# Optimization experiments

Measured on AMD Instinct MI355X. Metric: run time of the kernel, lower is better.

The kernel has to match this reference:

```python
import jax, jax.numpy as jnp
import numpy as np

NUM_EXPERTS = 8
HIDDEN = 2048
INTER = 4096
TOKENS = 8192
TOP_K = 2


def setup_inputs() -> dict:
    key = jax.random.key(0)
    ks = jax.random.split(key, 5)
    s = 0.02
    return {
        "x": jax.random.normal(ks[0], (TOKENS, HIDDEN), dtype=jnp.float32),
        "gate_w": jax.random.normal(ks[1], (NUM_EXPERTS, HIDDEN), dtype=jnp.float32) * s,
        "w1": jax.random.normal(ks[2], (NUM_EXPERTS, INTER, HIDDEN), dtype=jnp.float32) * s,
        "w2": jax.random.normal(ks[3], (NUM_EXPERTS, HIDDEN, INTER), dtype=jnp.float32) * s,
        "w3": jax.random.normal(ks[4], (NUM_EXPERTS, INTER, HIDDEN), dtype=jnp.float32) * s,
    }


def reference(x, gate_w, w1, w2, w3):
    # Router: softmax over experts in fp32, then top-2 (no renormalization,
    # matching the torch module which uses the raw top-k softmax probs).
    router_logits = jnp.einsum("th,eh->te", x, gate_w)  # [T, E]
    probs = jax.nn.softmax(router_logits.astype(jnp.float32), axis=1)
    topk_w, topk_idx = jax.lax.top_k(probs, TOP_K)  # [T, K]
    topk_w = topk_w.astype(x.dtype)

    num_experts = w1.shape[0]
    out = jnp.zeros_like(x)
    for e in range(num_experts):
        # Combined routing coefficient for expert e per token (0 if unrouted).
        coef = jnp.sum(jnp.where(topk_idx == e, topk_w, 0.0), axis=1)  # [T]
        # SwiGLU expert FFN: down(silu(gate(x)) * up(x))
        g = jnp.einsum("th,ih->ti", x, w1[e])
        u = jnp.einsum("th,ih->ti", x, w3[e])
        h = jax.nn.silu(g) * u
        y = jnp.einsum("ti,hi->th", h, w2[e])
        out = out + coef[:, None] * y
    return out
```

## Files before the change

kernel.cpp:

```cpp
#include <hip/hip_runtime.h>
#include <stdint.h>
#include <stddef.h>


constexpr int kTokens  = 8192;
constexpr int kHidden  = 2048;
constexpr int kInter   = 4096;
constexpr int kExperts = 8;

constexpr int BM = 128;
constexpr int BN = 128;
constexpr int BK = 64;
constexpr int MAX_MT = (2 * kTokens) / BM + kExperts;

typedef short bf16x8 __attribute__((ext_vector_type(8)));
typedef float f32x4  __attribute__((ext_vector_type(4)));
typedef unsigned int u32;

__device__ __forceinline__ unsigned short f2bf(float f) {
  union { float f; unsigned u; } v; v.f = f;
  unsigned r = v.u + 0x7FFFu + ((v.u >> 16) & 1u);
  return (unsigned short)(r >> 16);
}

__device__ __forceinline__ void gload16(const void* g, void* l) {
  __builtin_amdgcn_global_load_lds(
      (const __attribute__((address_space(1))) u32*)g,
      (__attribute__((address_space(3))) u32*)l, 16, 0, 0);
}

__global__ __launch_bounds__(256) void convert_w(
    const float* __restrict__ src, unsigned short* __restrict__ dst,
    int lp, int lq, int K, long nchunks)
{
  long stride = (long)gridDim.x * blockDim.x;
  for (long g = blockIdx.x * (long)blockDim.x + threadIdx.x; g < nchunks; g += stride) {
    int  l   = (int)(g & 1023);
    long blk = g >> 10;
    int  q   = (int)(blk & ((1 << lq) - 1));
    long ep  = blk >> lq;
    int  p   = (int)(ep & ((1 << lp) - 1));
    int  e   = (int)(ep >> lp);
    int r = l >> 3, cs = l & 7, c = cs ^ (r & 7);
    size_t soff = (((size_t)(e << lp) + p) * 128 + r) * (size_t)K + (size_t)q * 64 + c * 8;
    float4 v0 = *reinterpret_cast<const float4*>(src + soff);
    float4 v1 = *reinterpret_cast<const float4*>(src + soff + 4);
    uint4 o;
    o.x = (u32)f2bf(v0.x) | ((u32)f2bf(v0.y) << 16);
    o.y = (u32)f2bf(v0.z) | ((u32)f2bf(v0.w) << 16);
    o.z = (u32)f2bf(v1.x) | ((u32)f2bf(v1.y) << 16);
    o.w = (u32)f2bf(v1.z) | ((u32)f2bf(v1.w) << 16);
    *reinterpret_cast<uint4*>(dst + g * 8) = o;
  }
}

__global__ __launch_bounds__(256) void moe_router(
    const float* __restrict__ x, const float* __restrict__ gate_w,
    unsigned short* __restrict__ xb, int* __restrict__ counts,
    int* __restrict__ list_idx, float* __restrict__ list_w)
{
  const int lane = threadIdx.x & 63;
  const int wave = threadIdx.x >> 6;
  const int t = blockIdx.x * 4 + wave;

  float acc[kExperts];
#pragma unroll
  for (int e = 0; e < kExperts; ++e) acc[e] = 0.f;

  const float4* xrow = reinterpret_cast<const float4*>(x + (size_t)t * kHidden);
#pragma unroll
  for (int j = 0; j < 8; ++j) {
    float4 xv = xrow[j * 64 + lane];
    uint2 pk;
    pk.x = (u32)f2bf(xv.x) | ((u32)f2bf(xv.y) << 16);
    pk.y = (u32)f2bf(xv.z) | ((u32)f2bf(xv.w) << 16);
    *reinterpret_cast<uint2*>(xb + (size_t)t * kHidden + j * 256 + lane * 4) = pk;
#pragma unroll
    for (int e = 0; e < kExperts; ++e) {
      float4 gv = reinterpret_cast<const float4*>(gate_w + (size_t)e * kHidden)[j * 64 + lane];
      acc[e] += xv.x * gv.x + xv.y * gv.y + xv.z * gv.z + xv.w * gv.w;
    }
  }
#pragma unroll
  for (int e = 0; e < kExperts; ++e) {
#pragma unroll
    for (int m = 32; m >= 1; m >>= 1) acc[e] += __shfl_xor(acc[e], m);
  }
  if (lane == 0) {
    float mx = acc[0];
#pragma unroll
    for (int e = 1; e < kExperts; ++e) mx = fmaxf(mx, acc[e]);
    float p[kExperts]; float s = 0.f;
#pragma unroll
    for (int e = 0; e < kExperts; ++e) { p[e] = __expf(acc[e] - mx); s += p[e]; }
    float inv = 1.f / s;
    int i1 = 0; float v1 = p[0];
#pragma unroll
    for (int e = 1; e < kExperts; ++e) if (p[e] > v1) { v1 = p[e]; i1 = e; }
    int i2 = (i1 == 0) ? 1 : 0; float v2 = p[i2];
#pragma unroll
    for (int e = 0; e < kExperts; ++e) {
      if (e == i1 || e == i2) continue;
      if (p[e] > v2) { v2 = p[e]; i2 = e; }
    }
    int s1 = atomicAdd(&counts[i1], 1);
    list_idx[i1 * kTokens + s1] = t;
    list_w [i1 * kTokens + s1] = v1 * inv;
    int s2 = atomicAdd(&counts[i2], 1);
    list_idx[i2 * kTokens + s2] = t;
    list_w [i2 * kTokens + s2] = v2 * inv;
  }
}

__device__ __forceinline__ bool map_tile(const int* __restrict__ counts, int mt,
                                         int& e, int& lm, int& sb, int& ne)
{
  int tb = 0; sb = 0;
  for (e = 0; e < kExperts; ++e) {
    ne = counts[e];
    int tiles = (ne + BM - 1) / BM;
    if (mt < tb + tiles) { lm = mt - tb; return true; }
    tb += tiles; sb += ne;
  }
  return false;
}

__global__ __launch_bounds__(256, 2) void moe_gu(
    const unsigned short* __restrict__ xb,
    const unsigned short* __restrict__ w1b, const unsigned short* __restrict__ w3b,
    const int* __restrict__ counts, const int* __restrict__ list_idx,
    unsigned short* __restrict__ hbuf)
{
  __shared__ unsigned short As [BM * BK];
  __shared__ unsigned short B1s[BN * BK];
  __shared__ unsigned short B3s[BN * BK];
  __shared__ int toks[BM];

  const int tid = threadIdx.x;
  const int nt  = blockIdx.x / MAX_MT;
  const int mt  = blockIdx.x % MAX_MT;

  int e, lm, sb, ne;
  if (!map_tile(counts, mt, e, lm, sb, ne)) return;
  const int row0 = lm * BM;

  if (tid < BM) {
    int lr = row0 + tid;
    toks[tid] = list_idx[e * kTokens + ((lr < ne) ? lr : 0)];
  }
  __syncthreads();

  const int lane = tid & 63;
  const int w = tid >> 6;
  const int wr = w >> 1, wc = w & 1;

  const unsigned short* srcA[4];
  const unsigned short* srcB1[4];
  const unsigned short* srcB3[4];
  const size_t bbase = ((size_t)(e * (kInter / BN) + nt) * (kHidden / BK)) * 1024;
#pragma unroll
  for (int i = 0; i < 4; ++i) {
    int l = (w * 4 + i) * 64 + lane;
    int r = l >> 3, cs = l & 7, c = cs ^ (r & 7);
    srcA[i]  = xb  + (size_t)toks[r] * kHidden + c * 8;
    srcB1[i] = w1b + (bbase + l) * 8;
    srcB3[i] = w3b + (bbase + l) * 8;
  }

  f32x4 accG[4][4], accU[4][4];
  const f32x4 zero = {0.f, 0.f, 0.f, 0.f};
#pragma unroll
  for (int m = 0; m < 4; ++m)
#pragma unroll
    for (int n = 0; n < 4; ++n) { accG[m][n] = zero; accU[m][n] = zero; }

  for (int ks = 0; ks < kHidden / BK; ++ks) {
#pragma unroll
    for (int i = 0; i < 4; ++i) {
      gload16(srcA[i]  + ks * BK,            &As [(w * 4 + i) * 512]);
      gload16(srcB1[i] + (size_t)ks * 8192,  &B1s[(w * 4 + i) * 512]);
      gload16(srcB3[i] + (size_t)ks * 8192,  &B3s[(w * 4 + i) * 512]);
    }
    __syncthreads();
#pragma unroll
    for (int kk = 0; kk < 2; ++kk) {
      const int cq = kk * 4 + (lane >> 4);
      bf16x8 a[4], b1v[4], b3v[4];
#pragma unroll
      for (int m = 0; m < 4; ++m) {
        int row = wr * 64 + m * 16 + (lane & 15);
        a[m] = *reinterpret_cast<const bf16x8*>(&As[row * 64 + ((cq ^ (row & 7)) << 3)]);
      }
#pragma unroll
      for (int n = 0; n < 4; ++n) {
        int row = wc * 64 + n * 16 + (lane & 15);
        b1v[n] = *reinterpret_cast<const bf16x8*>(&B1s[row * 64 + ((cq ^ (row & 7)) << 3)]);
        b3v[n] = *reinterpret_cast<const bf16x8*>(&B3s[row * 64 + ((cq ^ (row & 7)) << 3)]);
      }
#pragma unroll
      for (int m = 0; m < 4; ++m)
#pragma unroll
        for (int n = 0; n < 4; ++n) {
          accG[m][n] = __builtin_amdgcn_mfma_f32_16x16x32_bf16(a[m], b1v[n], accG[m][n], 0, 0, 0);
          accU[m][n] = __builtin_amdgcn_mfma_f32_16x16x32_bf16(a[m], b3v[n], accU[m][n], 0, 0, 0);
        }
    }
    __syncthreads();
  }

#pragma unroll
  for (int m = 0; m < 4; ++m) {
#pragma unroll
    for (int r = 0; r < 4; ++r) {
      int rloc = wr * 64 + m * 16 + ((lane >> 4) * 4) + r;
      int lrow = row0 + rloc;
      if (lrow < ne) {
        size_t base = (size_t)(sb + lrow) * kInter + (size_t)nt * BN + wc * 64 + (lane & 15);
#pragma unroll
        for (int n = 0; n < 4; ++n) {
          float g = accG[m][n][r];
          float u = accU[m][n][r];
          float hv = (g / (1.f + __expf(-g))) * u;
          hbuf[base + n * 16] = f2bf(hv);
        }
      }
    }
  }
}

__global__ __launch_bounds__(256, 3) void moe_y(
    const unsigned short* __restrict__ hbuf,
    const unsigned short* __restrict__ w2b,
    const int* __restrict__ counts, const int* __restrict__ list_idx,
    const float* __restrict__ list_w,
    float* __restrict__ out)
{
  __shared__ unsigned short As[BM * BK];
  __shared__ unsigned short Bs[BN * BK];
  __shared__ int   toks[BM];
  __shared__ float cofs[BM];

  const int tid = threadIdx.x;
  const int nt  = blockIdx.x / MAX_MT;
  const int mt  = blockIdx.x % MAX_MT;

  int e, lm, sb, ne;
  if (!map_tile(counts, mt, e, lm, sb, ne)) return;
  const int row0 = lm * BM;

  if (tid < BM) {
    int lr = row0 + tid;
    bool v = lr < ne;
    toks[tid] = v ? list_idx[e * kTokens + lr] : 0;
    cofs[tid] = v ? list_w [e * kTokens + lr] : 0.f;
  }
  __syncthreads();

  const int lane = tid & 63;
  const int w = tid >> 6;
  const int wr = w >> 1, wc = w & 1;

  const unsigned short* srcA[4];
  const unsigned short* srcB2[4];
  const size_t bbase = ((size_t)(e * (kHidden / BN) + nt) * (kInter / BK)) * 1024;
#pragma unroll
  for (int i = 0; i < 4; ++i) {
    int l = (w * 4 + i) * 64 + lane;
    int r = l >> 3, cs = l & 7, c = cs ^ (r & 7);
    srcA[i]  = hbuf + (size_t)(sb + row0 + r) * kInter + c * 8;
    srcB2[i] = w2b  + (bbase + l) * 8;
  }

  f32x4 acc[4][4];
  const f32x4 zero = {0.f, 0.f, 0.f, 0.f};
#pragma unroll
  for (int m = 0; m < 4; ++m)
#pragma unroll
    for (int n = 0; n < 4; ++n) acc[m][n] = zero;

  for (int ks = 0; ks < kInter / BK; ++ks) {
#pragma unroll
    for (int i = 0; i < 4; ++i) {
      gload16(srcA[i]  + ks * BK,           &As[(w * 4 + i) * 512]);
      gload16(srcB2[i] + (size_t)ks * 8192, &Bs[(w * 4 + i) * 512]);
    }
    __syncthreads();
#pragma unroll
    for (int kk = 0; kk < 2; ++kk) {
      const int cq = kk * 4 + (lane >> 4);
      bf16x8 a[4], b[4];
#pragma unroll
      for (int m = 0; m < 4; ++m) {
        int row = wr * 64 + m * 16 + (lane & 15);
        a[m] = *reinterpret_cast<const bf16x8*>(&As[row * 64 + ((cq ^ (row & 7)) << 3)]);
      }
#pragma unroll
      for (int n = 0; n < 4; ++n) {
        int row = wc * 64 + n * 16 + (lane & 15);
        b[n] = *reinterpret_cast<const bf16x8*>(&Bs[row * 64 + ((cq ^ (row & 7)) << 3)]);
      }
#pragma unroll
      for (int m = 0; m < 4; ++m)
#pragma unroll
        for (int n = 0; n < 4; ++n)
          acc[m][n] = __builtin_amdgcn_mfma_f32_16x16x32_bf16(a[m], b[n], acc[m][n], 0, 0, 0);
    }
    __syncthreads();
  }

#pragma unroll
  for (int m = 0; m < 4; ++m) {
#pragma unroll
    for (int r = 0; r < 4; ++r) {
      int rloc = wr * 64 + m * 16 + ((lane >> 4) * 4) + r;
      if (row0 + rloc < ne) {
        float cf = cofs[rloc];
        size_t obase = (size_t)toks[rloc] * kHidden + (size_t)nt * BN + wc * 64 + (lane & 15);
#pragma unroll
        for (int n = 0; n < 4; ++n)
          atomicAdd(&out[obase + n * 16], cf * acc[m][n][r]);
      }
    }
  }
}

__global__ __launch_bounds__(256, 2) void moe_gu_f32(
    const unsigned short* __restrict__ xb,
    const float* __restrict__ w1, const float* __restrict__ w3,
    const int* __restrict__ counts, const int* __restrict__ list_idx,
    unsigned short* __restrict__ hbuf)
{
  __shared__ unsigned short As [BM * BK];
  __shared__ unsigned short B1s[BN * BK];
  __shared__ unsigned short B3s[BN * BK];
  __shared__ int toks[BM];

  const int tid = threadIdx.x;
  const int nt  = blockIdx.x / MAX_MT;
  const int mt  = blockIdx.x % MAX_MT;

  int e, lm, sb, ne;
  if (!map_tile(counts, mt, e, lm, sb, ne)) return;
  const int row0 = lm * BM;

  if (tid < BM) {
    int lr = row0 + tid;
    toks[tid] = list_idx[e * kTokens + ((lr < ne) ? lr : 0)];
  }
  __syncthreads();

  const unsigned short* aptr[4];
#pragma unroll
  for (int i = 0; i < 4; ++i) {
    int chunk = i * 256 + tid;
    int r = chunk >> 3, c8 = chunk & 7;
    aptr[i] = xb + (size_t)toks[r] * kHidden + c8 * 8;
  }
  const float* w1e = w1 + (size_t)e * kInter * kHidden;
  const float* w3e = w3 + (size_t)e * kInter * kHidden;

  f32x4 accG[4][4], accU[4][4];
  const f32x4 zero = {0.f, 0.f, 0.f, 0.f};
#pragma unroll
  for (int m = 0; m < 4; ++m)
#pragma unroll
    for (int n = 0; n < 4; ++n) { accG[m][n] = zero; accU[m][n] = zero; }

  const int lane = tid & 63;
  const int wr = (tid >> 6) >> 1;
  const int wc = (tid >> 6) & 1;

  for (int k0 = 0; k0 < kHidden; k0 += BK) {
#pragma unroll
    for (int i = 0; i < 4; ++i) {
      int chunk = i * 256 + tid;
      uint4 v = *reinterpret_cast<const uint4*>(aptr[i] + k0);
      *reinterpret_cast<uint4*>(&As[chunk * 8]) = v;
    }
#pragma unroll
    for (int i = 0; i < 8; ++i) {
      int c = i * 256 + tid;
      int rowB = c >> 4, c16 = c & 15;
      size_t off = ((size_t)(nt * BN + rowB)) * kHidden + k0 + c16 * 4;
      float4 v1 = *reinterpret_cast<const float4*>(w1e + off);
      float4 v3 = *reinterpret_cast<const float4*>(w3e + off);
      uint2 p1, p3;
      p1.x = (u32)f2bf(v1.x) | ((u32)f2bf(v1.y) << 16);
      p1.y = (u32)f2bf(v1.z) | ((u32)f2bf(v1.w) << 16);
      p3.x = (u32)f2bf(v3.x) | ((u32)f2bf(v3.y) << 16);
      p3.y = (u32)f2bf(v3.z) | ((u32)f2bf(v3.w) << 16);
      *reinterpret_cast<uint2*>(&B1s[rowB * BK + c16 * 4]) = p1;
      *reinterpret_cast<uint2*>(&B3s[rowB * BK + c16 * 4]) = p3;
    }
    __syncthreads();
#pragma unroll
    for (int kk = 0; kk < 2; ++kk) {
      const int klo = kk * 32 + (lane >> 4) * 8;
      bf16x8 a[4], b1v[4], b3v[4];
#pragma unroll
      for (int m = 0; m < 4; ++m)
        a[m] = *reinterpret_cast<const bf16x8*>(&As[(wr * 64 + m * 16 + (lane & 15)) * BK + klo]);
#pragma unroll
      for (int n = 0; n < 4; ++n) {
        b1v[n] = *reinterpret_cast<const bf16x8*>(&B1s[(wc * 64 + n * 16 + (lane & 15)) * BK + klo]);
        b3v[n] = *reinterpret_cast<const bf16x8*>(&B3s[(wc * 64 + n * 16 + (lane & 15)) * BK + klo]);
      }
#pragma unroll
      for (int m = 0; m < 4; ++m)
#pragma unroll
        for (int n = 0; n < 4; ++n) {
          accG[m][n] = __builtin_amdgcn_mfma_f32_16x16x32_bf16(a[m], b1v[n], accG[m][n], 0, 0, 0);
          accU[m][n] = __builtin_amdgcn_mfma_f32_16x16x32_bf16(a[m], b3v[n], accU[m][n], 0, 0, 0);
        }
    }
    __syncthreads();
  }
#pragma unroll
  for (int m = 0; m < 4; ++m) {
#pragma unroll
    for (int r = 0; r < 4; ++r) {
      int rloc = wr * 64 + m * 16 + ((lane >> 4) * 4) + r;
      int lrow = row0 + rloc;
      if (lrow < ne) {
        size_t base = (size_t)(sb + lrow) * kInter + (size_t)nt * BN + wc * 64 + (lane & 15);
#pragma unroll
        for (int n = 0; n < 4; ++n) {
          float g = accG[m][n][r];
          float u = accU[m][n][r];
          hbuf[base + n * 16] = f2bf((g / (1.f + __expf(-g))) * u);
        }
      }
    }
  }
}

__global__ __launch_bounds__(256, 2) void moe_y_f32(
    const unsigned short* __restrict__ hbuf,
    const float* __restrict__ w2,
    const int* __restrict__ counts, const int* __restrict__ list_idx,
    const float* __restrict__ list_w,
    float* __restrict__ out)
{
  __shared__ unsigned short As[BM * BK];
  __shared__ unsigned short Bs[BN * BK];
  __shared__ int   toks[BM];
  __shared__ float cofs[BM];

  const int tid = threadIdx.x;
  const int nt  = blockIdx.x / MAX_MT;
  const int mt  = blockIdx.x % MAX_MT;

  int e, lm, sb, ne;
  if (!map_tile(counts, mt, e, lm, sb, ne)) return;
  const int row0 = lm * BM;

  if (tid < BM) {
    int lr = row0 + tid;
    bool v = lr < ne;
    toks[tid] = v ? list_idx[e * kTokens + lr] : 0;
    cofs[tid] = v ? list_w [e * kTokens + lr] : 0.f;
  }
  __syncthreads();

  const float* w2e = w2 + (size_t)e * kHidden * kInter;
  const unsigned short* arow = hbuf + (size_t)(sb + row0) * kInter;

  f32x4 acc[4][4];
  const f32x4 zero = {0.f, 0.f, 0.f, 0.f};
#pragma unroll
  for (int m = 0; m < 4; ++m)
#pragma unroll
    for (int n = 0; n < 4; ++n) acc[m][n] = zero;

  const int lane = tid & 63;
  const int wr = (tid >> 6) >> 1;
  const int wc = (tid >> 6) & 1;

  for (int k0 = 0; k0 < kInter; k0 += BK) {
#pragma unroll
    for (int i = 0; i < 4; ++i) {
      int chunk = i * 256 + tid;
      int r = chunk >> 3, c8 = chunk & 7;
      uint4 v = *reinterpret_cast<const uint4*>(arow + (size_t)r * kInter + k0 + c8 * 8);
      *reinterpret_cast<uint4*>(&As[chunk * 8]) = v;
    }
#pragma unroll
    for (int i = 0; i < 8; ++i) {
      int c = i * 256 + tid;
      int rowB = c >> 4, c16 = c & 15;
      size_t off = ((size_t)(nt * BN + rowB)) * kInter + k0 + c16 * 4;
      float4 v2 = *reinterpret_cast<const float4*>(w2e + off);
      uint2 p2;
      p2.x = (u32)f2bf(v2.x) | ((u32)f2bf(v2.y) << 16);
      p2.y = (u32)f2bf(v2.z) | ((u32)f2bf(v2.w) << 16);
      *reinterpret_cast<uint2*>(&Bs[rowB * BK + c16 * 4]) = p2;
    }
    __syncthreads();
#pragma unroll
    for (int kk = 0; kk < 2; ++kk) {
      const int klo = kk * 32 + (lane >> 4) * 8;
      bf16x8 a[4], b[4];
#pragma unroll
      for (int m = 0; m < 4; ++m)
        a[m] = *reinterpret_cast<const bf16x8*>(&As[(wr * 64 + m * 16 + (lane & 15)) * BK + klo]);
#pragma unroll
      for (int n = 0; n < 4; ++n)
        b[n] = *reinterpret_cast<const bf16x8*>(&Bs[(wc * 64 + n * 16 + (lane & 15)) * BK + klo]);
#pragma unroll
      for (int m = 0; m < 4; ++m)
#pragma unroll
        for (int n = 0; n < 4; ++n)
          acc[m][n] = __builtin_amdgcn_mfma_f32_16x16x32_bf16(a[m], b[n], acc[m][n], 0, 0, 0);
    }
    __syncthreads();
  }
#pragma unroll
  for (int m = 0; m < 4; ++m) {
#pragma unroll
    for (int r = 0; r < 4; ++r) {
      int rloc = wr * 64 + m * 16 + ((lane >> 4) * 4) + r;
      if (row0 + rloc < ne) {
        float cf = cofs[rloc];
        size_t obase = (size_t)toks[rloc] * kHidden + (size_t)nt * BN + wc * 64 + (lane & 15);
#pragma unroll
        for (int n = 0; n < 4; ++n)
          atomicAdd(&out[obase + n * 16], cf * acc[m][n][r]);
      }
    }
  }
}

extern "C" void kernel_launch(void* const* d_in, const int* in_sizes, int n_in,
                              void* d_out, int out_size, void* d_ws, size_t ws_size,
                              hipStream_t stream)
{
  const float* x      = (const float*)d_in[0];
  const float* gate_w = (const float*)d_in[1];
  const float* w1     = (const float*)d_in[2];
  const float* w2     = (const float*)d_in[3];
  const float* w3     = (const float*)d_in[4];
  float* out = (float*)d_out;

  char* ws = (char*)d_ws;
  const size_t MiB = 1ull << 20;
  int*   counts   = (int*)(ws);
  int*   list_idx = (int*)(ws + 1024);
  float* list_w   = (float*)(ws + 1024 + kExperts * kTokens * 4);

  hipMemsetAsync(counts, 0, 1024, stream);
  hipMemsetAsync(out, 0, (size_t)kTokens * kHidden * sizeof(float), stream);

  if (ws_size >= 418 * MiB) {
    unsigned short* xb   = (unsigned short*)(ws + 1 * MiB);
    unsigned short* w1b  = (unsigned short*)(ws + 33 * MiB);
    unsigned short* w3b  = (unsigned short*)(ws + 161 * MiB);
    unsigned short* hbuf = (unsigned short*)(ws + 289 * MiB);
    unsigned short* w2b  = w1b;

    const long nch = (long)kExperts * (kInter / BN) * (kHidden / BK) * 1024;
    convert_w<<<4096, 256, 0, stream>>>(w1, w1b, 5, 5, kHidden, nch);
    convert_w<<<4096, 256, 0, stream>>>(w3, w3b, 5, 5, kHidden, nch);
    moe_router<<<kTokens / 4, 256, 0, stream>>>(x, gate_w, xb, counts, list_idx, list_w);
    moe_gu<<<(kInter / BN) * MAX_MT, 256, 0, stream>>>(xb, w1b, w3b, counts, list_idx, hbuf);
    convert_w<<<4096, 256, 0, stream>>>(w2, w2b, 4, 6, kInter, nch);
    moe_y<<<(kHidden / BN) * MAX_MT, 256, 0, stream>>>(hbuf, w2b, counts, list_idx, list_w, out);
  } else {
    unsigned short* xb   = (unsigned short*)(ws + 1 * MiB);
    unsigned short* hbuf = (unsigned short*)(ws + 36 * MiB);
    moe_router<<<kTokens / 4, 256, 0, stream>>>(x, gate_w, xb, counts, list_idx, list_w);
    moe_gu_f32<<<(kInter / BN) * MAX_MT, 256, 0, stream>>>(xb, w1, w3, counts, list_idx, hbuf);
    moe_y_f32 <<<(kHidden / BN) * MAX_MT, 256, 0, stream>>>(hbuf, w2, counts, list_idx, list_w, out);
  }
}
```

Baseline: 1.498 ms.

## Rewrite gate/up GEMM as 256-row tile, 8-wave double-buffered ping-pong kernel

Replaces the gate/up expert GEMM with a 512-thread kernel that uses 256x128 tiles and double-buffers A, W1 and W3 tiles in 128KB of LDS. Global-to-LDS loads for the next K step are interleaved with MFMA phases, using s_setprio, explicit vmcnt waits and split barriers. The aim is to hide load latency and raise arithmetic intensity per block. The cost is higher LDS use, which limits occupancy, and tail waste on smaller per-expert tiles. The fine-grained waitcnt counts must stay correct.

```diff
diff --git a/kernel.cpp b/kernel.cpp
--- a/kernel.cpp
+++ b/kernel.cpp
@@ -8,10 +8,12 @@
 constexpr int kInter   = 4096;
 constexpr int kExperts = 8;
 
-constexpr int BM = 128;
-constexpr int BN = 128;
-constexpr int BK = 64;
+constexpr int BM = 128, BN = 128, BK = 64;
 constexpr int MAX_MT = (2 * kTokens) / BM + kExperts;
+
+constexpr int BM2 = 256, BN2 = 128, BK2 = 64;
+constexpr int MAX_MT2 = (2 * kTokens) / BM2 + kExperts;
+constexpr int NT2 = kHidden / BK2;
 
 typedef short bf16x8 __attribute__((ext_vector_type(8)));
 typedef float f32x4  __attribute__((ext_vector_type(4)));
@@ -125,101 +127,207 @@
   return false;
 }
 
-__global__ __launch_bounds__(256, 2) void moe_gu(
+__device__ __forceinline__ bool map_tile2(const int* __restrict__ counts, int mt,
+                                          int& e, int& lm, int& sb, int& ne)
+{
+  int tb = 0; sb = 0;
+  for (e = 0; e < kExperts; ++e) {
+    ne = counts[e];
+    int tiles = (ne + BM2 - 1) / BM2;
+    if (mt < tb + tiles) { lm = mt - tb; return true; }
+    tb += tiles; sb += ne;
+  }
+  return false;
+}
+
+__global__ __launch_bounds__(512, 2) void moe_gu2(
     const unsigned short* __restrict__ xb,
     const unsigned short* __restrict__ w1b, const unsigned short* __restrict__ w3b,
     const int* __restrict__ counts, const int* __restrict__ list_idx,
     unsigned short* __restrict__ hbuf)
 {
-  __shared__ unsigned short As [BM * BK];
-  __shared__ unsigned short B1s[BN * BK];
-  __shared__ unsigned short B3s[BN * BK];
-  __shared__ int toks[BM];
+  __shared__ unsigned short lds[65536];
+  __shared__ int toks[BM2];
 
   const int tid = threadIdx.x;
-  const int nt  = blockIdx.x / MAX_MT;
-  const int mt  = blockIdx.x % MAX_MT;
+  const int nt  = blockIdx.x / MAX_MT2;
+  const int mt  = blockIdx.x % MAX_MT2;
 
   int e, lm, sb, ne;
-  if (!map_tile(counts, mt, e, lm, sb, ne)) return;
-  const int row0 = lm * BM;
-
-  if (tid < BM) {
+  if (!map_tile2(counts, mt, e, lm, sb, ne)) return;
+  const int row0 = lm * BM2;
+
+  if (tid < BM2) {
     int lr = row0 + tid;
     toks[tid] = list_idx[e * kTokens + ((lr < ne) ? lr : 0)];
   }
   __syncthreads();
 
   const int lane = tid & 63;
-  const int w = tid >> 6;
-  const int wr = w >> 1, wc = w & 1;
-
-  const unsigned short* srcA[4];
-  const unsigned short* srcB1[4];
-  const unsigned short* srcB3[4];
-  const size_t bbase = ((size_t)(e * (kInter / BN) + nt) * (kHidden / BK)) * 1024;
-#pragma unroll
-  for (int i = 0; i < 4; ++i) {
-    int l = (w * 4 + i) * 64 + lane;
-    int r = l >> 3, cs = l & 7, c = cs ^ (r & 7);
-    srcA[i]  = xb  + (size_t)toks[r] * kHidden + c * 8;
-    srcB1[i] = w1b + (bbase + l) * 8;
-    srcB3[i] = w3b + (bbase + l) * 8;
-  }
-
-  f32x4 accG[4][4], accU[4][4];
+  const int w    = tid >> 6;
+  const int wr   = w >> 2;
+  const int wc   = w & 3;
+
+  const unsigned short* srcA[2][2];
+  const unsigned short* srcB1[2];
+  const unsigned short* srcB3[2];
+  {
+    const size_t bb = ((size_t)(e * (kInter / BN2) + nt) * (kHidden / BK2)) * 1024;
+#pragma unroll
+    for (int i = 0; i < 2; ++i) {
+      int l = (w * 2 + i) * 64 + lane;
+      int r = l >> 3, cs = l & 7, c = cs ^ (r & 7);
+#pragma unroll
+      for (int h = 0; h < 2; ++h)
+        srcA[h][i] = xb + (size_t)toks[h * 128 + r] * kHidden + c * 8;
+      srcB1[i] = w1b + (bb + l) * 8;
+      srcB3[i] = w3b + (bb + l) * 8;
+    }
+  }
+
+  f32x4 accG[8][2], accU[8][2];
   const f32x4 zero = {0.f, 0.f, 0.f, 0.f};
 #pragma unroll
-  for (int m = 0; m < 4; ++m)
-#pragma unroll
-    for (int n = 0; n < 4; ++n) { accG[m][n] = zero; accU[m][n] = zero; }
-
-  for (int ks = 0; ks < kHidden / BK; ++ks) {
-#pragma unroll
-    for (int i = 0; i < 4; ++i) {
-      gload16(srcA[i]  + ks * BK,            &As [(w * 4 + i) * 512]);
-      gload16(srcB1[i] + (size_t)ks * 8192,  &B1s[(w * 4 + i) * 512]);
-      gload16(srcB3[i] + (size_t)ks * 8192,  &B3s[(w * 4 + i) * 512]);
-    }
-    __syncthreads();
-#pragma unroll
-    for (int kk = 0; kk < 2; ++kk) {
-      const int cq = kk * 4 + (lane >> 4);
-      bf16x8 a[4], b1v[4], b3v[4];
+  for (int m = 0; m < 8; ++m)
+#pragma unroll
+    for (int n = 0; n < 2; ++n) { accG[m][n] = zero; accU[m][n] = zero; }
+
+#pragma unroll
+  for (int i = 0; i < 2; ++i) gload16(srcA[0][i], &lds[0 * 8192 + (w * 2 + i) * 512]);
+#pragma unroll
+  for (int i = 0; i < 2; ++i) gload16(srcA[1][i], &lds[1 * 8192 + (w * 2 + i) * 512]);
+#pragma unroll
+  for (int i = 0; i < 2; ++i) gload16(srcB1[i], &lds[32768 + (w * 2 + i) * 512]);
+#pragma unroll
+  for (int i = 0; i < 2; ++i) gload16(srcB3[i], &lds[49152 + (w * 2 + i) * 512]);
+  asm volatile("s_waitcnt vmcnt(2)" ::: "memory");
+  __builtin_amdgcn_sched_barrier(0);
+  __builtin_amdgcn_s_barrier();
+
+  for (int t = 0; t < NT2; ++t) {
+    const int cb = t & 1, nb = cb ^ 1;
+    const int tn = (t + 1 < NT2) ? (t + 1) : (NT2 - 1);
+    const int Acur = (cb * 2 + wr) * 8192;
+    const int B1c  = 32768 + cb * 8192;
+    const int B3c  = 49152 + cb * 8192;
+    const int An0  = (nb * 2 + 0) * 8192;
+    const int An1  = (nb * 2 + 1) * 8192;
+    const int B1n  = 32768 + nb * 8192;
+    const int B3n  = 49152 + nb * 8192;
+
+    bf16x8 a0[4][2], a1[4][2];
+    {
+      bf16x8 b1f[2][2];
 #pragma unroll
       for (int m = 0; m < 4; ++m) {
-        int row = wr * 64 + m * 16 + (lane & 15);
-        a[m] = *reinterpret_cast<const bf16x8*>(&As[row * 64 + ((cq ^ (row & 7)) << 3)]);
-      }
-#pragma unroll
-      for (int n = 0; n < 4; ++n) {
-        int row = wc * 64 + n * 16 + (lane & 15);
-        b1v[n] = *reinterpret_cast<const bf16x8*>(&B1s[row * 64 + ((cq ^ (row & 7)) << 3)]);
-        b3v[n] = *reinterpret_cast<const bf16x8*>(&B3s[row * 64 + ((cq ^ (row & 7)) << 3)]);
-      }
-#pragma unroll
-      for (int m = 0; m < 4; ++m)
-#pragma unroll
-        for (int n = 0; n < 4; ++n) {
-          accG[m][n] = __builtin_amdgcn_mfma_f32_16x16x32_bf16(a[m], b1v[n], accG[m][n], 0, 0, 0);
-          accU[m][n] = __builtin_amdgcn_mfma_f32_16x16x32_bf16(a[m], b3v[n], accU[m][n], 0, 0, 0);
+        const int r = m * 16 + (lane & 15);
+#pragma unroll
+        for (int kk = 0; kk < 2; ++kk) {
+          const int cq = kk * 4 + (lane >> 4);
+          a0[m][kk] = *reinterpret_cast<const bf16x8*>(&lds[Acur + r * 64 + ((cq ^ (r & 7)) << 3)]);
         }
-    }
-    __syncthreads();
-  }
-
-#pragma unroll
-  for (int m = 0; m < 4; ++m) {
+      }
+#pragma unroll
+      for (int n = 0; n < 2; ++n) {
+        const int r = wc * 32 + n * 16 + (lane & 15);
+#pragma unroll
+        for (int kk = 0; kk < 2; ++kk) {
+          const int cq = kk * 4 + (lane >> 4);
+          b1f[n][kk] = *reinterpret_cast<const bf16x8*>(&lds[B1c + r * 64 + ((cq ^ (r & 7)) << 3)]);
+        }
+      }
+#pragma unroll
+      for (int i = 0; i < 2; ++i) gload16(srcA[0][i] + tn * 64, &lds[An0 + (w * 2 + i) * 512]);
+      __builtin_amdgcn_s_setprio(1);
+#pragma unroll
+      for (int m = 0; m < 4; ++m)
+#pragma unroll
+        for (int n = 0; n < 2; ++n)
+#pragma unroll
+          for (int kk = 0; kk < 2; ++kk)
+            accG[m][n] = __builtin_amdgcn_mfma_f32_16x16x32_bf16(a0[m][kk], b1f[n][kk], accG[m][n], 0, 0, 0);
+      __builtin_amdgcn_s_setprio(0);
+      __builtin_amdgcn_sched_barrier(0);
+      __builtin_amdgcn_s_barrier();
+
+#pragma unroll
+      for (int m = 0; m < 4; ++m) {
+        const int r = 64 + m * 16 + (lane & 15);
+#pragma unroll
+        for (int kk = 0; kk < 2; ++kk) {
+          const int cq = kk * 4 + (lane >> 4);
+          a1[m][kk] = *reinterpret_cast<const bf16x8*>(&lds[Acur + r * 64 + ((cq ^ (r & 7)) << 3)]);
+        }
+      }
+#pragma unroll
+      for (int i = 0; i < 2; ++i) gload16(srcA[1][i] + tn * 64, &lds[An1 + (w * 2 + i) * 512]);
+      __builtin_amdgcn_s_setprio(1);
+#pragma unroll
+      for (int m = 0; m < 4; ++m)
+#pragma unroll
+        for (int n = 0; n < 2; ++n)
+#pragma unroll
+          for (int kk = 0; kk < 2; ++kk)
+            accG[4 + m][n] = __builtin_amdgcn_mfma_f32_16x16x32_bf16(a1[m][kk], b1f[n][kk], accG[4 + m][n], 0, 0, 0);
+      __builtin_amdgcn_s_setprio(0);
+      __builtin_amdgcn_sched_barrier(0);
+      asm volatile("s_waitcnt vmcnt(4)" ::: "memory");
+      __builtin_amdgcn_s_barrier();
+    }
+    {
+      bf16x8 b3f[2][2];
+#pragma unroll
+      for (int n = 0; n < 2; ++n) {
+        const int r = wc * 32 + n * 16 + (lane & 15);
+#pragma unroll
+        for (int kk = 0; kk < 2; ++kk) {
+          const int cq = kk * 4 + (lane >> 4);
+          b3f[n][kk] = *reinterpret_cast<const bf16x8*>(&lds[B3c + r * 64 + ((cq ^ (r & 7)) << 3)]);
+        }
+      }
+#pragma unroll
+      for (int i = 0; i < 2; ++i) gload16(srcB1[i] + (size_t)tn * 8192, &lds[B1n + (w * 2 + i) * 512]);
+      __builtin_amdgcn_s_setprio(1);
+#pragma unroll
+      for (int m = 0; m < 4; ++m)
+#pragma unroll
+        for (int n = 0; n < 2; ++n)
+#pragma unroll
+          for (int kk = 0; kk < 2; ++kk)
+            accU[m][n] = __builtin_amdgcn_mfma_f32_16x16x32_bf16(a0[m][kk], b3f[n][kk], accU[m][n], 0, 0, 0);
+      __builtin_amdgcn_s_setprio(0);
+      __builtin_amdgcn_sched_barrier(0);
+      __builtin_amdgcn_s_barrier();
+
+#pragma unroll
+      for (int i = 0; i < 2; ++i) gload16(srcB3[i] + (size_t)tn * 8192, &lds[B3n + (w * 2 + i) * 512]);
+      __builtin_amdgcn_s_setprio(1);
+#pragma unroll
+      for (int m = 0; m < 4; ++m)
+#pragma unroll
+        for (int n = 0; n < 2; ++n)
+#pragma unroll
+          for (int kk = 0; kk < 2; ++kk)
+            accU[4 + m][n] = __builtin_amdgcn_mfma_f32_16x16x32_bf16(a1[m][kk], b3f[n][kk], accU[4 + m][n], 0, 0, 0);
+      __builtin_amdgcn_s_setprio(0);
+      __builtin_amdgcn_sched_barrier(0);
+      asm volatile("s_waitcnt vmcnt(2)" ::: "memory");
+      __builtin_amdgcn_s_barrier();
+    }
+  }
+
+#pragma unroll
+  for (int am = 0; am < 8; ++am) {
 #pragma unroll
     for (int r = 0; r < 4; ++r) {
-      int rloc = wr * 64 + m * 16 + ((lane >> 4) * 4) + r;
+      int rloc = wr * 128 + am * 16 + ((lane >> 4) * 4) + r;
       int lrow = row0 + rloc;
       if (lrow < ne) {
-        size_t base = (size_t)(sb + lrow) * kInter + (size_t)nt * BN + wc * 64 + (lane & 15);
-#pragma unroll
-        for (int n = 0; n < 4; ++n) {
-          float g = accG[m][n][r];
-          float u = accU[m][n][r];
+        size_t base = (size_t)(sb + lrow) * kInter + (size_t)nt * BN2 + wc * 32 + (lane & 15);
+#pragma unroll
+        for (int n = 0; n < 2; ++n) {
+          float g = accG[am][n][r];
+          float u = accU[am][n][r];
           float hv = (g / (1.f + __expf(-g))) * u;
           hbuf[base + n * 16] = f2bf(hv);
         }
@@ -561,7 +669,7 @@
     convert_w<<<4096, 256, 0, stream>>>(w1, w1b, 5, 5, kHidden, nch);
     convert_w<<<4096, 256, 0, stream>>>(w3, w3b, 5, 5, kHidden, nch);
     moe_router<<<kTokens / 4, 256, 0, stream>>>(x, gate_w, xb, counts, list_idx, list_w);
-    moe_gu<<<(kInter / BN) * MAX_MT, 256, 0, stream>>>(xb, w1b, w3b, counts, list_idx, hbuf);
+    moe_gu2<<<(kInter / BN2) * MAX_MT2, 512, 0, stream>>>(xb, w1b, w3b, counts, list_idx, hbuf);
     convert_w<<<4096, 256, 0, stream>>>(w2, w2b, 4, 6, kInter, nch);
     moe_y<<<(kHidden / BN) * MAX_MT, 256, 0, stream>>>(hbuf, w2b, counts, list_idx, list_w, out);
   } else {
```

Result: no change. 1.492 ms (-0.4%).

## Replace atomic scatter in down-proj with per-rank buffers, wider tiles and merge

Applied to the files above, without the earlier changes.

The router now packs each token's top-k rank into list_idx. The down-projection kernel writes coef-scaled outputs into two per-rank fp32 buffers instead of doing atomicAdd into the output, and a separate merge kernel sums the two buffers into out. The down-proj kernel now uses 512 threads with 256-wide N tiles, so each staged A tile is reused across twice as many output columns. This removes the output memset and the contended fp32 atomics, at the cost of an extra 128 MiB write plus read. ybuf reuses the w3b workspace region, which is safe because w3b is no longer needed at that point.

```diff
diff --git a/kernel.cpp b/kernel.cpp
--- a/kernel.cpp
+++ b/kernel.cpp
@@ -8,10 +8,11 @@
 constexpr int kInter   = 4096;
 constexpr int kExperts = 8;
 
-constexpr int BM = 128;
-constexpr int BN = 128;
-constexpr int BK = 64;
+constexpr int BM = 128, BN = 128, BK = 64;
 constexpr int MAX_MT = (2 * kTokens) / BM + kExperts;
+constexpr int NTY = kInter / BK;
+constexpr int NPAN_Y5 = kHidden / 256;
+constexpr int kSlotCap = 16512;
 
 typedef short bf16x8 __attribute__((ext_vector_type(8)));
 typedef float f32x4  __attribute__((ext_vector_type(4)));
@@ -104,10 +105,10 @@
       if (p[e] > v2) { v2 = p[e]; i2 = e; }
     }
     int s1 = atomicAdd(&counts[i1], 1);
-    list_idx[i1 * kTokens + s1] = t;
+    list_idx[i1 * kTokens + s1] = t * 2 + 0;
     list_w [i1 * kTokens + s1] = v1 * inv;
     int s2 = atomicAdd(&counts[i2], 1);
-    list_idx[i2 * kTokens + s2] = t;
+    list_idx[i2 * kTokens + s2] = t * 2 + 1;
     list_w [i2 * kTokens + s2] = v2 * inv;
   }
 }
@@ -146,7 +147,7 @@
 
   if (tid < BM) {
     int lr = row0 + tid;
-    toks[tid] = list_idx[e * kTokens + ((lr < ne) ? lr : 0)];
+    toks[tid] = list_idx[e * kTokens + ((lr < ne) ? lr : 0)] >> 1;
   }
   __syncthreads();
 
@@ -228,17 +229,18 @@
   }
 }
 
-__global__ __launch_bounds__(256, 3) void moe_y(
+__global__ __launch_bounds__(512, 4) void moe_y5(
     const unsigned short* __restrict__ hbuf,
     const unsigned short* __restrict__ w2b,
     const int* __restrict__ counts, const int* __restrict__ list_idx,
     const float* __restrict__ list_w,
-    float* __restrict__ out)
-{
-  __shared__ unsigned short As[BM * BK];
-  __shared__ unsigned short Bs[BN * BK];
+    float* __restrict__ ybuf)
+{
+  __shared__ unsigned short As[8192];
+  __shared__ unsigned short Bs[2][8192];
   __shared__ int   toks[BM];
   __shared__ float cofs[BM];
+  __shared__ int   rnks[BM];
 
   const int tid = threadIdx.x;
   const int nt  = blockIdx.x / MAX_MT;
@@ -251,25 +253,33 @@
   if (tid < BM) {
     int lr = row0 + tid;
     bool v = lr < ne;
-    toks[tid] = v ? list_idx[e * kTokens + lr] : 0;
-    cofs[tid] = v ? list_w [e * kTokens + lr] : 0.f;
+    int pk = v ? list_idx[e * kTokens + lr] : 0;
+    toks[tid] = pk >> 1;
+    rnks[tid] = pk & 1;
+    cofs[tid] = v ? list_w[e * kTokens + lr] : 0.f;
   }
   __syncthreads();
 
   const int lane = tid & 63;
-  const int w = tid >> 6;
-  const int wr = w >> 1, wc = w & 1;
-
-  const unsigned short* srcA[4];
-  const unsigned short* srcB2[4];
-  const size_t bbase = ((size_t)(e * (kHidden / BN) + nt) * (kInter / BK)) * 1024;
-#pragma unroll
-  for (int i = 0; i < 4; ++i) {
-    int l = (w * 4 + i) * 64 + lane;
-    int r = l >> 3, cs = l & 7, c = cs ^ (r & 7);
-    srcA[i]  = hbuf + (size_t)(sb + row0 + r) * kInter + c * 8;
-    srcB2[i] = w2b  + (bbase + l) * 8;
-  }
+  const int w    = tid >> 6;
+  const int wr   = w >> 2;
+  const int wc   = w & 3;
+
+  const unsigned short* srcA[2];
+  int cOff[2];
+#pragma unroll
+  for (int j = 0; j < 2; ++j) {
+    int l = (w * 2 + j) * 64 + lane;
+    int r = l >> 3, c = (l & 7) ^ (r & 7);
+    int rg = sb + row0 + r;
+    if (rg > kSlotCap - 1) rg = kSlotCap - 1;
+    srcA[j] = hbuf + (size_t)rg * kInter + c * 8;
+    cOff[j] = l * 8;
+  }
+  const unsigned short* pB[2];
+#pragma unroll
+  for (int h = 0; h < 2; ++h)
+    pB[h] = w2b + (size_t)(e * 16 + nt * 2 + h) * NTY * 8192;
 
   f32x4 acc[4][4];
   const f32x4 zero = {0.f, 0.f, 0.f, 0.f};
@@ -278,11 +288,12 @@
 #pragma unroll
     for (int n = 0; n < 4; ++n) acc[m][n] = zero;
 
-  for (int ks = 0; ks < kInter / BK; ++ks) {
-#pragma unroll
-    for (int i = 0; i < 4; ++i) {
-      gload16(srcA[i]  + ks * BK,           &As[(w * 4 + i) * 512]);
-      gload16(srcB2[i] + (size_t)ks * 8192, &Bs[(w * 4 + i) * 512]);
+  for (int ks = 0; ks < NTY; ++ks) {
+#pragma unroll
+    for (int j = 0; j < 2; ++j) {
+      gload16(srcA[j] + ks * BK, &As[(w * 2 + j) * 512]);
+      gload16(pB[0] + (size_t)ks * 8192 + cOff[j], &Bs[0][(w * 2 + j) * 512]);
+      gload16(pB[1] + (size_t)ks * 8192 + cOff[j], &Bs[1][(w * 2 + j) * 512]);
     }
     __syncthreads();
 #pragma unroll
@@ -296,8 +307,9 @@
       }
 #pragma unroll
       for (int n = 0; n < 4; ++n) {
-        int row = wc * 64 + n * 16 + (lane & 15);
-        b[n] = *reinterpret_cast<const bf16x8*>(&Bs[row * 64 + ((cq ^ (row & 7)) << 3)]);
+        int rr = wc * 64 + n * 16 + (lane & 15);
+        int h = rr >> 7, rl = rr & 127;
+        b[n] = *reinterpret_cast<const bf16x8*>(&Bs[h][rl * 64 + ((cq ^ (rl & 7)) << 3)]);
       }
 #pragma unroll
       for (int m = 0; m < 4; ++m)
@@ -315,12 +327,25 @@
       int rloc = wr * 64 + m * 16 + ((lane >> 4) * 4) + r;
       if (row0 + rloc < ne) {
         float cf = cofs[rloc];
-        size_t obase = (size_t)toks[rloc] * kHidden + (size_t)nt * BN + wc * 64 + (lane & 15);
+        size_t obase = ((size_t)rnks[rloc] * kTokens + toks[rloc]) * kHidden
+                     + (size_t)nt * 256 + wc * 64 + (lane & 15);
 #pragma unroll
         for (int n = 0; n < 4; ++n)
-          atomicAdd(&out[obase + n * 16], cf * acc[m][n][r]);
-      }
-    }
+          ybuf[obase + n * 16] = cf * acc[m][n][r];
+      }
+    }
+  }
+}
+
+__global__ __launch_bounds__(256) void moe_merge(
+    const float4* __restrict__ y0, const float4* __restrict__ y1,
+    float4* __restrict__ out, int n4)
+{
+  int stride = gridDim.x * blockDim.x;
+  for (int i = blockIdx.x * blockDim.x + threadIdx.x; i < n4; i += stride) {
+    float4 a = y0[i], b = y1[i];
+    float4 o; o.x = a.x + b.x; o.y = a.y + b.y; o.z = a.z + b.z; o.w = a.w + b.w;
+    out[i] = o;
   }
 }
 
@@ -345,7 +370,7 @@
 
   if (tid < BM) {
     int lr = row0 + tid;
-    toks[tid] = list_idx[e * kTokens + ((lr < ne) ? lr : 0)];
+    toks[tid] = list_idx[e * kTokens + ((lr < ne) ? lr : 0)] >> 1;
   }
   __syncthreads();
 
@@ -457,7 +482,7 @@
   if (tid < BM) {
     int lr = row0 + tid;
     bool v = lr < ne;
-    toks[tid] = v ? list_idx[e * kTokens + lr] : 0;
+    toks[tid] = v ? (list_idx[e * kTokens + lr] >> 1) : 0;
     cofs[tid] = v ? list_w [e * kTokens + lr] : 0.f;
   }
   __syncthreads();
@@ -548,7 +573,6 @@
   float* list_w   = (float*)(ws + 1024 + kExperts * kTokens * 4);
 
   hipMemsetAsync(counts, 0, 1024, stream);
-  hipMemsetAsync(out, 0, (size_t)kTokens * kHidden * sizeof(float), stream);
 
   if (ws_size >= 418 * MiB) {
     unsigned short* xb   = (unsigned short*)(ws + 1 * MiB);
@@ -556,17 +580,22 @@
     unsigned short* w3b  = (unsigned short*)(ws + 161 * MiB);
     unsigned short* hbuf = (unsigned short*)(ws + 289 * MiB);
     unsigned short* w2b  = w1b;
-
-    const long nch = (long)kExperts * (kInter / BN) * (kHidden / BK) * 1024;
+    float*          ybuf = (float*)(ws + 161 * MiB);
+
+    const long nch = (long)kExperts * 32 * 32 * 1024;
     convert_w<<<4096, 256, 0, stream>>>(w1, w1b, 5, 5, kHidden, nch);
     convert_w<<<4096, 256, 0, stream>>>(w3, w3b, 5, 5, kHidden, nch);
     moe_router<<<kTokens / 4, 256, 0, stream>>>(x, gate_w, xb, counts, list_idx, list_w);
     moe_gu<<<(kInter / BN) * MAX_MT, 256, 0, stream>>>(xb, w1b, w3b, counts, list_idx, hbuf);
     convert_w<<<4096, 256, 0, stream>>>(w2, w2b, 4, 6, kInter, nch);
-    moe_y<<<(kHidden / BN) * MAX_MT, 256, 0, stream>>>(hbuf, w2b, counts, list_idx, list_w, out);
+    moe_y5<<<NPAN_Y5 * MAX_MT, 512, 0, stream>>>(hbuf, w2b, counts, list_idx, list_w, ybuf);
+    moe_merge<<<2048, 256, 0, stream>>>(
+        (const float4*)ybuf, (const float4*)(ybuf + (size_t)kTokens * kHidden),
+        (float4*)out, kTokens * kHidden / 4);
   } else {
     unsigned short* xb   = (unsigned short*)(ws + 1 * MiB);
     unsigned short* hbuf = (unsigned short*)(ws + 36 * MiB);
+    hipMemsetAsync(out, 0, (size_t)kTokens * kHidden * sizeof(float), stream);
     moe_router<<<kTokens / 4, 256, 0, stream>>>(x, gate_w, xb, counts, list_idx, list_w);
     moe_gu_f32<<<(kInter / BN) * MAX_MT, 256, 0, stream>>>(xb, w1, w3, counts, list_idx, hbuf);
     moe_y_f32 <<<(kHidden / BN) * MAX_MT, 256, 0, stream>>>(hbuf, w2, counts, list_idx, list_w, out);
```

Result: faster. 1.444 ms (-3.6%).
